# Optimization experiments

Hardware: AMD Instinct MI355X
Metric: run time of the kernel (lower is better)

Reference implementation:

```python
import jax, jax.numpy as jnp
import numpy as np
from jax import lax

B, H, W, C = 8, 128, 128, 256
HEADS, WIN, PRETRAIN = 8, 8, 8
QK_U = C // HEADS            # 32
QK_CH = QK_U * HEADS         # 256
KV_CH = QK_CH + C            # 512
BLOCK = WIN // 2             # key block size at half resolution
HALO = WIN                   # halo window (halo_window//2) at half resolution
PAD = (HALO - BLOCK) // 2    # halo overlap pad at half resolution


def _win_part(x, heads):
    b, h, w, c = x.shape
    u = c // heads
    x = x.reshape(b, h // WIN, WIN, w // WIN, WIN, heads, u)
    x = x.transpose(0, 1, 3, 5, 2, 4, 6)
    return x.reshape(b, (h // WIN) * (w // WIN), heads, WIN * WIN, u)


def _halo_part(x):
    # overlapping halo blocks: [b,hh,wh,c] -> [b, nw, HALO*HALO, c]
    b, h, w, c = x.shape
    xp = jnp.pad(x, ((0, 0), (PAD, PAD), (PAD, PAD), (0, 0)))
    hb, wb = h // BLOCK, w // BLOCK
    ih = jnp.arange(hb)[:, None] * BLOCK + jnp.arange(HALO)[None, :]
    iw = jnp.arange(wb)[:, None] * BLOCK + jnp.arange(HALO)[None, :]
    t = xp[:, ih][:, :, :, iw]            # [b, hb, HALO, wb, HALO, c]
    t = t.transpose(0, 1, 3, 2, 4, 5)
    return t.reshape(b, hb * wb, HALO * HALO, c)


def _halo_part_fused(x, heads):
    t = _halo_part(x)
    b, nw, l, c = t.shape
    u = c // heads
    return t.reshape(b, nw, l, heads, u).transpose(0, 1, 3, 2, 4)


def _l2n(x):
    # tf.math.l2_normalize with epsilon=1.55e-5
    return x * lax.rsqrt(jnp.maximum(jnp.sum(x * x, -1, keepdims=True), 1.55e-5))


def _rel_bias(cpb_w1, cpb_b1, cpb_w2):
    # Swin-V2 style continuous (log-CPB) relative bias between full-res query
    # window and half-res halo key window.
    qc = jnp.arange(WIN, dtype=jnp.float32)
    kc = (jnp.arange(HALO, dtype=jnp.float32) - PAD) * 2.0 + 0.5  # half-res centers in full-res coords
    r1 = qc[:, None] - kc[None, :]
    rel_y = jnp.broadcast_to(r1[:, None, :, None], (WIN, WIN, HALO, HALO))
    rel_x = jnp.broadcast_to(r1[None, :, None, :], (WIN, WIN, HALO, HALO))
    rel = jnp.stack([rel_y, rel_x], -1).reshape(WIN * WIN, HALO * HALO, 2)
    rel = rel / (PRETRAIN - 1) * 8.0
    rel = jnp.sign(rel) * jnp.log2(jnp.abs(rel) + 1.0) / np.float32(np.log2(8.0))
    hmid = jax.nn.relu(rel @ cpb_w1 + cpb_b1)
    bias = 16.0 * jax.nn.sigmoid(hmid @ cpb_w2)   # [q, k, heads]
    return bias.transpose(2, 0, 1)[None, None]    # [1,1,heads,q,k]


def _pad_mask(dtype):
    # No outer divisible-pad here (H,W divisible), but halo zero-padding at the
    # image border must be masked out (-100 on out-of-image key positions).
    m = jnp.ones((1, H // 2, W // 2, 1), dtype)   # min-pooled validity map (all ones)
    hm = _halo_part(m)                            # [1, nw, HALO*HALO, 1]; border halos -> 0
    return -100.0 * (hm[..., 0] == 0).astype(dtype)[:, :, None, None, :]  # [1,nw,1,1,k]


def reference(inputs, qkv_w, q_bias, v_bias, dw_w, dw_gamma, dw_beta, dw_mean, dw_var, scale, cpb_w1, cpb_b1, cpb_w2, proj_w, proj_b):
    qkv = jnp.einsum('bhwc,cd->bhwd', inputs, qkv_w)
    q, kv = qkv[..., :QK_CH], qkv[..., QK_CH:]
    # depthwise 3x3 stride-2 conv + (inference) batch-norm on K/V path
    kv = lax.conv_general_dilated(kv, dw_w, (2, 2), 'SAME',
                                  dimension_numbers=('NHWC', 'HWIO', 'NHWC'),
                                  feature_group_count=KV_CH)
    kv = (kv - dw_mean) * lax.rsqrt(dw_var + 1e-3) * dw_gamma + dw_beta
    q = q + q_bias
    kv = kv + jnp.concatenate([jnp.zeros_like(q_bias), v_bias])
    qw = _win_part(q, HEADS)                                 # [B,nw,h,64,QK_U]
    k = _halo_part_fused(kv[..., :QK_CH], HEADS)             # [B,nw,h,64,QK_U]
    v = _halo_part_fused(kv[..., QK_CH:], HEADS)             # [B,nw,h,64,V_U]
    logit_scale = jnp.exp(jnp.minimum(scale, np.float32(np.log(100.0))))  # [h,1,1]
    attn = jnp.einsum('bnhqd,bnhkd->bnhqk', _l2n(qw) * logit_scale, _l2n(k))
    attn = attn + _rel_bias(cpb_w1, cpb_b1, cpb_w2) + _pad_mask(attn.dtype)
    attn = jax.nn.softmax(attn, axis=-1)
    out = jnp.einsum('bnhqk,bnhkd->bnhqd', attn, v)
    hb, wb = H // WIN, W // WIN
    out = out.reshape(B, hb, wb, HEADS, WIN, WIN, C // HEADS)
    out = out.transpose(0, 1, 4, 2, 5, 3, 6).reshape(B, H, W, C)
    return jnp.einsum('bhwc,cd->bhwd', out, proj_w) + proj_b


def setup_inputs() -> dict:
    key = jax.random.key(0)
    ks = jax.random.split(key, 16)
    rn = lambda k, s, sc=0.05: jax.random.normal(k, s, jnp.float32) * sc
    return {
        'inputs': jax.random.normal(ks[0], (B, H, W, C), jnp.float32),
        'qkv_w': rn(ks[1], (C, 2 * QK_CH + C)),
        'q_bias': rn(ks[2], (QK_CH,)),
        'v_bias': rn(ks[3], (C,)),
        'dw_w': rn(ks[4], (3, 3, 1, KV_CH)),
        'dw_gamma': 1.0 + rn(ks[5], (KV_CH,)),
        'dw_beta': rn(ks[6], (KV_CH,)),
        'dw_mean': rn(ks[7], (KV_CH,)),
        'dw_var': jax.random.uniform(ks[8], (KV_CH,), jnp.float32, 0.5, 1.5),
        'scale': jnp.full((HEADS, 1, 1), np.log(10.0), jnp.float32),
        'cpb_w1': rn(ks[9], (2, 512), 0.5),
        'cpb_b1': rn(ks[10], (512,), 0.1),
        'cpb_w2': rn(ks[11], (512, HEADS), 0.1),
        'proj_w': rn(ks[12], (C, C)),
        'proj_b': rn(ks[13], (C,)),
    }
```

## Files before the change

kernel.cpp:

```cpp
#include <hip/hip_runtime.h>
#include <stdint.h>


typedef __attribute__((ext_vector_type(8))) short short8;
typedef __attribute__((ext_vector_type(4))) short short4v;
typedef __attribute__((ext_vector_type(4))) float f32x4;

__device__ __forceinline__ float bf2f(unsigned short u){
  union { unsigned int i; float f; } x; x.i = ((unsigned int)u)<<16; return x.f;
}
__device__ __forceinline__ unsigned short f2bf(float f){
  union { float f; unsigned int i; } x; x.f = f;
  unsigned int r = x.i + 0x7FFFu + ((x.i>>16)&1u);
  return (unsigned short)(r>>16);
}
__device__ __forceinline__ void gl_lds16(const void* g, void* l){
  __builtin_amdgcn_global_load_lds((const __attribute__((address_space(1))) unsigned int*)g,
                                   (__attribute__((address_space(3))) unsigned int*)l, 16, 0, 0);
}

__global__ __launch_bounds__(256) void cvt_bf16_kernel(const float* __restrict__ in,
                                                       short* __restrict__ out, long n8)
{
  long stride = (long)gridDim.x * 256;
  for (long i = (long)blockIdx.x*256 + threadIdx.x; i < n8; i += stride){
    float4 a = ((const float4*)in)[2*i];
    float4 b = ((const float4*)in)[2*i+1];
    short8 v;
    v[0]=(short)f2bf(a.x); v[1]=(short)f2bf(a.y); v[2]=(short)f2bf(a.z); v[3]=(short)f2bf(a.w);
    v[4]=(short)f2bf(b.x); v[5]=(short)f2bf(b.y); v[6]=(short)f2bf(b.z); v[7]=(short)f2bf(b.w);
    ((short8*)out)[i] = v;
  }
}

__global__ void transpose_w_kernel(const float* __restrict__ w, short* __restrict__ wt,
                                   int K, int N)
{
  int idx = blockIdx.x*256 + threadIdx.x;
  if (idx >= K*N) return;
  int n = idx / K, k = idx - n*K;
  wt[idx] = (short)f2bf(w[(long)k*N + n]);
}

__global__ __launch_bounds__(64) void relbias_kernel(const float* __restrict__ w1,
    const float* __restrict__ b1, const float* __restrict__ w2, float* __restrict__ out)
{
  int q = blockIdx.x;
  int k = threadIdx.x;
  float ry = (float)(q>>3) - (((float)(k>>3) - 2.f)*2.f + 0.5f);
  float rx = (float)(q&7)  - (((float)(k&7)  - 2.f)*2.f + 0.5f);
  ry *= (8.f/7.f); rx *= (8.f/7.f);
  float sy = (ry>0.f)?1.f:((ry<0.f)?-1.f:0.f);
  float sx = (rx>0.f)?1.f:((rx<0.f)?-1.f:0.f);
  ry = sy * log2f(fabsf(ry)+1.f) * (1.f/3.f);
  rx = sx * log2f(fabsf(rx)+1.f) * (1.f/3.f);
  float acc[8] = {0,0,0,0,0,0,0,0};
  for (int j=0;j<512;j++){
    float hm = ry*w1[j] + rx*w1[512+j] + b1[j];
    hm = fmaxf(hm, 0.f);
#pragma unroll
    for (int h=0;h<8;h++) acc[h] += hm * w2[j*8+h];
  }
#pragma unroll
  for (int h=0;h<8;h++)
    out[h*4096 + q*64 + k] = 16.f / (1.f + __expf(-acc[h]));
}

template<int ND, int OUTMODE>
__global__ __launch_bounds__(256) void gemm_bt_kernel(const short* __restrict__ A,
    const short* __restrict__ Bt, const float* __restrict__ bias,
    short* __restrict__ out_q, short* __restrict__ out_kv, float* __restrict__ out_f)
{
  __shared__ short smem[32768];
  const int tid  = threadIdx.x;
  const int lane = tid & 63;
  const int wid  = tid >> 6;
  const int wr = wid >> 1, wc = wid & 1;

  constexpr int NCB = ND / 128;
  const int bid = blockIdx.x;
  const int xcd = bid & 7;
  const int idx = bid >> 3;
  const long row0 = (long)(xcd * 128 + idx / NCB) * 128;
  const int  col0 = (idx % NCB) * 128;

  f32x4 acc[4][4];
#pragma unroll
  for (int m=0;m<4;m++)
#pragma unroll
    for (int n=0;n<4;n++) acc[m][n] = (f32x4){0.f,0.f,0.f,0.f};

  auto stage = [&](int buf, int kt){
#pragma unroll
    for (int j = 0; j < 4; j++) {
      int f = j*256 + tid;
      int r = f >> 3, p = f & 7;
      gl_lds16(A + (row0 + r)*256 + kt + ((p ^ (r&7))<<3),
               smem + buf*8192 + ((j*256 + (wid<<6))<<3));
      gl_lds16(Bt + (long)(col0 + r)*256 + kt + ((p ^ (r&7))<<3),
               smem + 16384 + buf*8192 + ((j*256 + (wid<<6))<<3));
    }
  };
  auto compute = [&](int buf){
    const short* As = smem + buf*8192;
    const short* Bs = smem + 16384 + buf*8192;
#pragma unroll
    for (int ks = 0; ks < 2; ks++) {
      short8 af[4], bfv[4];
#pragma unroll
      for (int m=0;m<4;m++){
        int r = wr*64 + m*16 + (lane & 15);
        int g = ks*4 + (lane >> 4);
        af[m] = *(const short8*)(As + r*64 + ((g ^ (r&7))<<3));
      }
#pragma unroll
      for (int n=0;n<4;n++){
        int r = wc*64 + n*16 + (lane & 15);
        int g = ks*4 + (lane >> 4);
        bfv[n] = *(const short8*)(Bs + r*64 + ((g ^ (r&7))<<3));
      }
#pragma unroll
      for (int m=0;m<4;m++)
#pragma unroll
        for (int n=0;n<4;n++)
          acc[m][n] = __builtin_amdgcn_mfma_f32_16x16x32_bf16(af[m], bfv[n], acc[m][n], 0, 0, 0);
    }
  };

  stage(0, 0);
  __syncthreads();
#pragma unroll
  for (int t = 0; t < 4; t++){
    if (t < 3) stage((t+1)&1, (t+1)*64);
    compute(t&1);
    __syncthreads();
  }

  if (OUTMODE == 0) {
    float bcol[4];
#pragma unroll
    for (int n=0;n<4;n++){
      int col = col0 + wc*64 + n*16 + (lane&15);
      bcol[n] = (col < 256) ? bias[col] : 0.f;
    }
#pragma unroll
    for (int m=0;m<4;m++){
#pragma unroll
      for (int n=0;n<4;n++){
        int col = wc*64 + n*16 + (lane&15);
        int cg = col >> 3;
#pragma unroll
        for (int rg=0;rg<4;rg++){
          int row = wr*64 + m*16 + ((lane>>4)<<2) + rg;
          smem[row*128 + ((cg ^ (row&7))<<3) + (col&7)] = (short)f2bf(acc[m][n][rg] + bcol[n]);
        }
      }
    }
    __syncthreads();
    int row = tid >> 1, ch = tid & 1;
    long grow = row0 + row;
#pragma unroll
    for (int j=0;j<8;j++){
      int cg = ch*8 + j;
      short8 v = *(const short8*)(smem + row*128 + ((cg ^ (row&7))<<3));
      int col = col0 + cg*8;
      if (col0 < 256) *(short8*)(out_q + grow*256 + col)        = v;
      else            *(short8*)(out_kv + grow*512 + (col-256)) = v;
    }
  } else {
    float* fs = (float*)smem;
#pragma unroll
    for (int m=0;m<4;m++){
#pragma unroll
      for (int n=0;n<4;n++){
        int col = wc*64 + n*16 + (lane&15);
        int c4 = col >> 2;
        float bv = bias[col0 + col];
#pragma unroll
        for (int rg=0;rg<4;rg++){
          int row = wr*64 + m*16 + ((lane>>4)<<2) + rg;
          fs[row*128 + ((c4 ^ (row&7))<<2) + (col&3)] = acc[m][n][rg] + bv;
        }
      }
    }
    __syncthreads();
    int row = tid >> 1;
    long grow = row0 + row;
#pragma unroll
    for (int j=0;j<16;j++){
      int c4 = (tid&1)*16 + j;
      float4 v = *(const float4*)(fs + row*128 + ((c4 ^ (row&7))<<2));
      *(float4*)(out_f + grow*ND + col0 + c4*4) = v;
    }
  }
}

__global__ __launch_bounds__(256) void dwconv_kernel(const short* __restrict__ kv_buf,
    const float* __restrict__ dw_w, const float* __restrict__ gamma,
    const float* __restrict__ beta, const float* __restrict__ mean,
    const float* __restrict__ var, const float* __restrict__ v_bias,
    short* __restrict__ kv_ds)
{
  const int bid = blockIdx.x;
  const int b  = bid >> 7;
  const int rem = bid & 127;
  const int y2 = rem >> 1, xq = rem & 1;
  const int tid = threadIdx.x;
  const int lane = tid & 63, w = tid >> 6;
  const int ch0 = lane * 8;

  float s[8], sh[8];
#pragma unroll
  for (int i=0;i<8;i+=4){
    float4 g4 = *(const float4*)(gamma + ch0 + i);
    float4 v4 = *(const float4*)(var   + ch0 + i);
    float4 m4 = *(const float4*)(mean  + ch0 + i);
    float4 b4 = *(const float4*)(beta  + ch0 + i);
    float gg[4] = {g4.x,g4.y,g4.z,g4.w}, vv[4] = {v4.x,v4.y,v4.z,v4.w};
    float mm[4] = {m4.x,m4.y,m4.z,m4.w}, bb[4] = {b4.x,b4.y,b4.z,b4.w};
#pragma unroll
    for (int j=0;j<4;j++){
      float sv = gg[j] * rsqrtf(vv[j] + 1e-3f);
      s[i+j]  = sv;
      sh[i+j] = bb[j] - mm[j]*sv;
    }
  }
  if (ch0 >= 256){
    float4 vb0 = *(const float4*)(v_bias + ch0 - 256);
    float4 vb1 = *(const float4*)(v_bias + ch0 - 252);
    sh[0]+=vb0.x; sh[1]+=vb0.y; sh[2]+=vb0.z; sh[3]+=vb0.w;
    sh[4]+=vb1.x; sh[5]+=vb1.y; sh[6]+=vb1.z; sh[7]+=vb1.w;
  }

  float wv[9][8];
#pragma unroll
  for (int t=0;t<9;t++){
    float4 w0 = *(const float4*)(dw_w + t*512 + ch0);
    float4 w1 = *(const float4*)(dw_w + t*512 + ch0 + 4);
    wv[t][0]=w0.x; wv[t][1]=w0.y; wv[t][2]=w0.z; wv[t][3]=w0.w;
    wv[t][4]=w1.x; wv[t][5]=w1.y; wv[t][6]=w1.z; wv[t][7]=w1.w;
  }

  const int y0 = y2*2;
  const bool vy2 = (y0 + 2) < 128;
  const short* r0 = kv_buf + (((long)b*128 + y0)*128)*512 + ch0;
  const short* r1 = r0 + 128*512;
  const short* r2 = r1 + 128*512;
  const short8 zero8 = {0,0,0,0,0,0,0,0};

  const int x2base = xq*32 + w*8;
  const int xs = x2base*2;

  auto ld = [&](const short* r, int x, bool vy)->short8 {
    if (vy && x < 128) return *(const short8*)(r + (long)x*512);
    return zero8;
  };

  short8 L0 = ld(r0, xs, true), L1 = ld(r1, xs, true), L2 = ld(r2, xs, vy2);

#pragma unroll
  for (int i=0;i<8;i++){
    const int x2 = x2base + i;
    const int xm = xs + 2*i + 1, xr = xs + 2*i + 2;
    short8 M0 = ld(r0, xm, true), M1 = ld(r1, xm, true), M2 = ld(r2, xm, vy2);
    short8 R0 = ld(r0, xr, true), R1 = ld(r1, xr, true), R2 = ld(r2, xr, vy2);

    float acc[8];
#pragma unroll
    for (int c=0;c<8;c++) acc[c] = 0.f;
#pragma unroll
    for (int c=0;c<8;c++){
      acc[c] += bf2f((unsigned short)L0[c]) * wv[0][c];
      acc[c] += bf2f((unsigned short)M0[c]) * wv[1][c];
      acc[c] += bf2f((unsigned short)R0[c]) * wv[2][c];
      acc[c] += bf2f((unsigned short)L1[c]) * wv[3][c];
      acc[c] += bf2f((unsigned short)M1[c]) * wv[4][c];
      acc[c] += bf2f((unsigned short)R1[c]) * wv[5][c];
      acc[c] += bf2f((unsigned short)L2[c]) * wv[6][c];
      acc[c] += bf2f((unsigned short)M2[c]) * wv[7][c];
      acc[c] += bf2f((unsigned short)R2[c]) * wv[8][c];
    }
    short8 o;
#pragma unroll
    for (int c=0;c<8;c++) o[c] = (short)f2bf(acc[c]*s[c] + sh[c]);
    *(short8*)(kv_ds + ((long)((b*64+y2)*64 + x2))*512 + ch0) = o;

    L0 = R0; L1 = R1; L2 = R2;
  }
}

__global__ __launch_bounds__(256) void halo_attn_kernel(const short* __restrict__ q_buf,
    const short* __restrict__ kv_ds, const float* __restrict__ relb,
    const float* __restrict__ scale, short* __restrict__ attn_out)
{
  __shared__ float qss[8][64];
  __shared__ float kss[8][64];
  __shared__ short vts[4][32][72];
  __shared__ short ps [4][64][72];

  const int bid = blockIdx.x;
  const int b = bid >> 8, wno = bid & 255;
  const int bi = wno >> 4, bj = wno & 15;
  const int tid = threadIdx.x;
  const int w = tid >> 6, lane = tid & 63;

#pragma unroll
  for (int i=0;i<4;i++){
    int idx = i*256 + tid;
    int isk = idx >> 9;
    int h   = (idx >> 6) & 7;
    int row = idx & 63;
    float ss = 0.f;
    if (!isk) {
      int qy = row>>3, qx = row&7;
      const short* p = q_buf + ((long)((b*128 + bi*8 + qy)*128 + (bj*8+qx)))*256 + h*32;
#pragma unroll
      for (int j=0;j<4;j++){
        short8 v = *(const short8*)(p + j*8);
#pragma unroll
        for (int e=0;e<8;e++){ float f = bf2f((unsigned short)v[e]); ss += f*f; }
      }
      qss[h][row] = fmaxf(ss, 1.55e-5f);
    } else {
      int ky = row>>3, kx = row&7;
      int yy = bi*4 - 2 + ky, xx = bj*4 - 2 + kx;
      if (yy>=0 && yy<64 && xx>=0 && xx<64) {
        const short* p = kv_ds + ((long)((b*64+yy)*64+xx))*512 + h*32;
#pragma unroll
        for (int j=0;j<4;j++){
          short8 v = *(const short8*)(p + j*8);
#pragma unroll
          for (int e=0;e<8;e++){ float f = bf2f((unsigned short)v[e]); ss += f*f; }
        }
      }
      kss[h][row] = fmaxf(ss, 1.55e-5f);
    }
  }
  __syncthreads();

  const short8 zero8 = {0,0,0,0,0,0,0,0};

  for (int hi=0; hi<2; hi++){
    int h = w + hi*4;
    float lscale = __expf(fminf(scale[h], 4.6051702f));

#pragma unroll 4
    for (int j=0;j<32;j++){
      int flat = j*64 + lane;
      int key = flat >> 5, d = flat & 31;
      int ky = key>>3, kx = key&7;
      int yy = bi*4-2+ky, xx = bj*4-2+kx;
      short val = 0;
      if (yy>=0 && yy<64 && xx>=0 && xx<64)
        val = kv_ds[((long)((b*64+yy)*64+xx))*512 + 256 + h*32 + d];
      vts[w][d][key] = val;
    }

    short8 af[4], bfv[4];
#pragma unroll
    for (int m=0;m<4;m++){
      int key = m*16 + (lane&15);
      int ky = key>>3, kx = key&7;
      int yy = bi*4-2+ky, xx = bj*4-2+kx;
      if (yy>=0 && yy<64 && xx>=0 && xx<64)
        af[m] = *(const short8*)(kv_ds + ((long)((b*64+yy)*64+xx))*512 + h*32 + ((lane>>4)<<3));
      else
        af[m] = zero8;
    }
#pragma unroll
    for (int n=0;n<4;n++){
      int q = n*16 + (lane&15);
      int qy = q>>3, qx = q&7;
      bfv[n] = *(const short8*)(q_buf + ((long)((b*128+bi*8+qy)*128 + bj*8+qx))*256 + h*32 + ((lane>>4)<<3));
    }
    f32x4 sc_[4][4];
#pragma unroll
    for (int m=0;m<4;m++)
#pragma unroll
      for (int n=0;n<4;n++)
        sc_[m][n] = __builtin_amdgcn_mfma_f32_16x16x32_bf16(af[m], bfv[n],
                        (f32x4){0.f,0.f,0.f,0.f}, 0, 0, 0);

    float rq[4];
#pragma unroll
    for (int n=0;n<4;n++) rq[n] = rsqrtf(qss[h][n*16 + (lane&15)]);
    float mx[4] = {-1e30f,-1e30f,-1e30f,-1e30f};
#pragma unroll
    for (int m=0;m<4;m++){
      int key0 = m*16 + ((lane>>4)<<2);
      float rk[4], mk[4];
#pragma unroll
      for (int r=0;r<4;r++){
        int key = key0 + r;
        int ky = key>>3, kx = key&7;
        int yy = bi*4-2+ky, xx = bj*4-2+kx;
        rk[r] = rsqrtf(kss[h][key]);
        mk[r] = (yy>=0 && yy<64 && xx>=0 && xx<64) ? 0.f : -100.f;
      }
#pragma unroll
      for (int n=0;n<4;n++){
        int q = n*16 + (lane&15);
        f32x4 rb = *(const f32x4*)(relb + h*4096 + q*64 + key0);
#pragma unroll
        for (int r=0;r<4;r++){
          float v = sc_[m][n][r] * (rk[r]*rq[n]*lscale) + rb[r] + mk[r];
          sc_[m][n][r] = v;
          mx[n] = fmaxf(mx[n], v);
        }
      }
    }
#pragma unroll
    for (int n=0;n<4;n++){
      mx[n] = fmaxf(mx[n], __shfl_xor(mx[n], 16));
      mx[n] = fmaxf(mx[n], __shfl_xor(mx[n], 32));
    }
    float sm[4] = {0.f,0.f,0.f,0.f};
#pragma unroll
    for (int m=0;m<4;m++)
#pragma unroll
      for (int n=0;n<4;n++)
#pragma unroll
        for (int r=0;r<4;r++){
          float e = __expf(sc_[m][n][r] - mx[n]);
          sc_[m][n][r] = e;
          sm[n] += e;
        }
#pragma unroll
    for (int n=0;n<4;n++){
      sm[n] += __shfl_xor(sm[n], 16);
      sm[n] += __shfl_xor(sm[n], 32);
      sm[n] = 1.f / sm[n];
    }
#pragma unroll
    for (int n=0;n<4;n++){
      int q = n*16 + (lane&15);
#pragma unroll
      for (int m=0;m<4;m++){
        short4v pk;
#pragma unroll
        for (int r=0;r<4;r++) pk[r] = (short)f2bf(sc_[m][n][r] * sm[n]);
        *(short4v*)(&ps[w][q][m*16 + ((lane>>4)<<2)]) = pk;
      }
    }
    __syncthreads();

    f32x4 oc[4][2];
#pragma unroll
    for (int m=0;m<4;m++)
#pragma unroll
      for (int n=0;n<2;n++) oc[m][n] = (f32x4){0.f,0.f,0.f,0.f};
#pragma unroll
    for (int ks=0; ks<2; ks++){
      short8 pa[4], vb[2];
#pragma unroll
      for (int m=0;m<4;m++)
        pa[m] = *(const short8*)(&ps[w][m*16 + (lane&15)][ks*32 + ((lane>>4)<<3)]);
#pragma unroll
      for (int n=0;n<2;n++)
        vb[n] = *(const short8*)(&vts[w][n*16 + (lane&15)][ks*32 + ((lane>>4)<<3)]);
#pragma unroll
      for (int m=0;m<4;m++)
#pragma unroll
        for (int n=0;n<2;n++)
          oc[m][n] = __builtin_amdgcn_mfma_f32_16x16x32_bf16(pa[m], vb[n], oc[m][n], 0, 0, 0);
    }
#pragma unroll
    for (int m=0;m<4;m++){
      int q0 = m*16 + ((lane>>4)<<2);
#pragma unroll
      for (int n=0;n<2;n++){
        int d = n*16 + (lane&15);
#pragma unroll
        for (int r=0;r<4;r++){
          int q = q0 + r;
          int qy = q>>3, qx = q&7;
          attn_out[((long)((b*128 + bi*8+qy)*128 + bj*8+qx))*256 + h*32 + d] =
              (short)f2bf(oc[m][n][r]);
        }
      }
    }
    __syncthreads();
  }
}

extern "C" void kernel_launch(void* const* d_in, const int* in_sizes, int n_in,
                              void* d_out, int out_size, void* d_ws, size_t ws_size,
                              hipStream_t stream)
{
  (void)in_sizes; (void)n_in; (void)out_size; (void)ws_size;
  const float* inputs = (const float*)d_in[0];
  const float* qkv_w  = (const float*)d_in[1];
  const float* q_bias = (const float*)d_in[2];
  const float* v_bias = (const float*)d_in[3];
  const float* dw_w   = (const float*)d_in[4];
  const float* dw_g   = (const float*)d_in[5];
  const float* dw_b   = (const float*)d_in[6];
  const float* dw_m   = (const float*)d_in[7];
  const float* dw_v   = (const float*)d_in[8];
  const float* scale  = (const float*)d_in[9];
  const float* cpb_w1 = (const float*)d_in[10];
  const float* cpb_b1 = (const float*)d_in[11];
  const float* cpb_w2 = (const float*)d_in[12];
  const float* proj_w = (const float*)d_in[13];
  const float* proj_b = (const float*)d_in[14];

  char* ws = (char*)d_ws;
  short* q_buf    = (short*)(ws);
  short* kv_buf   = (short*)(ws + 67108864L);
  short* kv_ds    = (short*)(ws + 201326592L);
  short* attn_buf = (short*)(ws + 234881024L);
  short* qkvw_t   = (short*)(ws + 301989888L);
  short* projw_t  = (short*)(ws + 302383104L);
  float* relb     = (float*)(ws + 302514176L);

  short* a_bf = attn_buf;

  cvt_bf16_kernel<<<2048, 256, 0, stream>>>(inputs, a_bf, 4194304L);
  transpose_w_kernel<<<768, 256, 0, stream>>>(qkv_w, qkvw_t, 256, 768);
  transpose_w_kernel<<<256, 256, 0, stream>>>(proj_w, projw_t, 256, 256);
  relbias_kernel<<<64, 64, 0, stream>>>(cpb_w1, cpb_b1, cpb_w2, relb);

  gemm_bt_kernel<768, 0><<<6144, 256, 0, stream>>>(
      a_bf, qkvw_t, q_bias, q_buf, kv_buf, nullptr);

  dwconv_kernel<<<1024, 256, 0, stream>>>(kv_buf, dw_w, dw_g, dw_b, dw_m, dw_v, v_bias, kv_ds);

  halo_attn_kernel<<<2048, 256, 0, stream>>>(q_buf, kv_ds, relb, scale, attn_buf);

  gemm_bt_kernel<256, 1><<<2048, 256, 0, stream>>>(
      attn_buf, projw_t, proj_b, nullptr, nullptr, (float*)d_out);
}
```

Before: 454.6 us.

## Store V transposed and padded, compute QK norms in-register in halo attention

The depthwise-conv kernel now writes K to its own compact buffer and V to a per-head, per-channel transposed plane padded by two pixels on each side. Halo attention can then load V fragments straight from global memory into MFMA operands, with no LDS staging and no bounds checks. The separate Q/K sum-of-squares pass and its LDS arrays are replaced by per-lane partial sums reduced with shuffles. Softmax uses exp2 with log2(e) folded into the scale and the relative bias, and normalization is deferred to the output. The P tile uses a per-wave swizzled LDS buffer without block barriers. The cost is scattered 2-byte V stores in dwconv, and the padded V border is never written, so correctness relies on the workspace already holding zeros there.

```diff
diff --git a/kernel.cpp b/kernel.cpp
--- a/kernel.cpp
+++ b/kernel.cpp
@@ -5,6 +5,8 @@
 typedef __attribute__((ext_vector_type(8))) short short8;
 typedef __attribute__((ext_vector_type(4))) short short4v;
 typedef __attribute__((ext_vector_type(4))) float f32x4;
+
+#define VT_PLANE 4624L
 
 __device__ __forceinline__ float bf2f(unsigned short u){
   union { unsigned int i; float f; } x; x.i = ((unsigned int)u)<<16; return x.f;
@@ -13,6 +15,10 @@
   union { float f; unsigned int i; } x; x.f = f;
   unsigned int r = x.i + 0x7FFFu + ((x.i>>16)&1u);
   return (unsigned short)(r>>16);
+}
+__device__ __forceinline__ unsigned int pack_bf_t(float a, float b){
+  union { float f; unsigned int u; } x, y; x.f = a; y.f = b;
+  return (y.u & 0xFFFF0000u) | (x.u >> 16);
 }
 __device__ __forceinline__ void gl_lds16(const void* g, void* l){
   __builtin_amdgcn_global_load_lds((const __attribute__((address_space(1))) unsigned int*)g,
@@ -63,7 +69,7 @@
   }
 #pragma unroll
   for (int h=0;h<8;h++)
-    out[h*4096 + q*64 + k] = 16.f / (1.f + __expf(-acc[h]));
+    out[h*4096 + q*64 + k] = (16.f / (1.f + __expf(-acc[h]))) * 1.4426950408889634f;
 }
 
 template<int ND, int OUTMODE>
@@ -199,7 +205,7 @@
     const float* __restrict__ dw_w, const float* __restrict__ gamma,
     const float* __restrict__ beta, const float* __restrict__ mean,
     const float* __restrict__ var, const float* __restrict__ v_bias,
-    short* __restrict__ kv_ds)
+    short* __restrict__ kv_K, short* __restrict__ v_t)
 {
   const int bid = blockIdx.x;
   const int b  = bid >> 7;
@@ -257,6 +263,9 @@
   };
 
   short8 L0 = ld(r0, xs, true), L1 = ld(r1, xs, true), L2 = ld(r2, xs, vy2);
+
+  const int vc = ch0 - 256, hh = vc >> 5, d0 = vc & 31;
+  const long vtb = ((long)((b*8+hh)*32 + d0))*VT_PLANE + (long)(y2+2)*68;
 
 #pragma unroll
   for (int i=0;i<8;i++){
@@ -283,128 +292,121 @@
     short8 o;
 #pragma unroll
     for (int c=0;c<8;c++) o[c] = (short)f2bf(acc[c]*s[c] + sh[c]);
-    *(short8*)(kv_ds + ((long)((b*64+y2)*64 + x2))*512 + ch0) = o;
-
+
+    if (ch0 < 256) {
+      *(short8*)(kv_K + ((long)((b*64+y2)*64 + x2))*256 + ch0) = o;
+    } else {
+      long base = vtb + (x2+2);
+#pragma unroll
+      for (int c=0;c<8;c++) v_t[base + (long)c*VT_PLANE] = o[c];
+    }
     L0 = R0; L1 = R1; L2 = R2;
   }
 }
 
 __global__ __launch_bounds__(256) void halo_attn_kernel(const short* __restrict__ q_buf,
-    const short* __restrict__ kv_ds, const float* __restrict__ relb,
-    const float* __restrict__ scale, short* __restrict__ attn_out)
-{
-  __shared__ float qss[8][64];
-  __shared__ float kss[8][64];
-  __shared__ short vts[4][32][72];
-  __shared__ short ps [4][64][72];
+    const short* __restrict__ kv_K, const short* __restrict__ v_t,
+    const float* __restrict__ relb, const float* __restrict__ scale,
+    short* __restrict__ attn_out)
+{
+  __shared__ short ps[4][4096];
 
   const int bid = blockIdx.x;
   const int b = bid >> 8, wno = bid & 255;
   const int bi = wno >> 4, bj = wno & 15;
   const int tid = threadIdx.x;
   const int w = tid >> 6, lane = tid & 63;
-
-#pragma unroll
-  for (int i=0;i<4;i++){
-    int idx = i*256 + tid;
-    int isk = idx >> 9;
-    int h   = (idx >> 6) & 7;
-    int row = idx & 63;
-    float ss = 0.f;
-    if (!isk) {
-      int qy = row>>3, qx = row&7;
-      const short* p = q_buf + ((long)((b*128 + bi*8 + qy)*128 + (bj*8+qx)))*256 + h*32;
-#pragma unroll
-      for (int j=0;j<4;j++){
-        short8 v = *(const short8*)(p + j*8);
-#pragma unroll
-        for (int e=0;e<8;e++){ float f = bf2f((unsigned short)v[e]); ss += f*f; }
-      }
-      qss[h][row] = fmaxf(ss, 1.55e-5f);
-    } else {
-      int ky = row>>3, kx = row&7;
-      int yy = bi*4 - 2 + ky, xx = bj*4 - 2 + kx;
-      if (yy>=0 && yy<64 && xx>=0 && xx<64) {
-        const short* p = kv_ds + ((long)((b*64+yy)*64+xx))*512 + h*32;
-#pragma unroll
-        for (int j=0;j<4;j++){
-          short8 v = *(const short8*)(p + j*8);
-#pragma unroll
-          for (int e=0;e<8;e++){ float f = bf2f((unsigned short)v[e]); ss += f*f; }
-        }
-      }
-      kss[h][row] = fmaxf(ss, 1.55e-5f);
-    }
-  }
-  __syncthreads();
-
+  const int g = lane >> 4, q15 = lane & 15;
+  short* myps = &ps[w][0];
   const short8 zero8 = {0,0,0,0,0,0,0,0};
 
+  long kbase[4]; bool kval[4];
+#pragma unroll
+  for (int m=0;m<4;m++){
+    int key = m*16 + q15;
+    int yy = bi*4-2 + (key>>3), xx = bj*4-2 + (key&7);
+    kval[m] = (yy>=0 && yy<64 && xx>=0 && xx<64);
+    kbase[m] = ((long)((b*64+yy)*64+xx))*256 + g*8;
+  }
+  float mkv[4][4];
+#pragma unroll
+  for (int m=0;m<4;m++)
+#pragma unroll
+    for (int r=0;r<4;r++){
+      int key = m*16 + g*4 + r;
+      int yy = bi*4-2+(key>>3), xx = bj*4-2+(key&7);
+      mkv[m][r] = (yy>=0&&yy<64&&xx>=0&&xx<64) ? 0.f : -30000.f;
+    }
+  long qpix[4];
+#pragma unroll
+  for (int n=0;n<4;n++){
+    int q = n*16+q15;
+    qpix[n] = ((long)((b*128+bi*8+(q>>3))*128 + bj*8+(q&7)))*256;
+  }
+  int voff[2];
+#pragma unroll
+  for (int ks=0;ks<2;ks++) voff[ks] = (bi*4+ks*4+g)*68 + bj*4;
+
   for (int hi=0; hi<2; hi++){
-    int h = w + hi*4;
-    float lscale = __expf(fminf(scale[h], 4.6051702f));
-
-#pragma unroll 4
-    for (int j=0;j<32;j++){
-      int flat = j*64 + lane;
-      int key = flat >> 5, d = flat & 31;
-      int ky = key>>3, kx = key&7;
-      int yy = bi*4-2+ky, xx = bj*4-2+kx;
-      short val = 0;
-      if (yy>=0 && yy<64 && xx>=0 && xx<64)
-        val = kv_ds[((long)((b*64+yy)*64+xx))*512 + 256 + h*32 + d];
-      vts[w][d][key] = val;
-    }
-
-    short8 af[4], bfv[4];
+    const int h = w + hi*4;
+    const float lsc = __expf(fminf(scale[h], 4.6051702f)) * 1.4426950408889634f;
+
+    short8 va[2][2];
+#pragma unroll
+    for (int dblk=0;dblk<2;dblk++){
+      long pl = ((long)((b*8+h)*32 + dblk*16 + q15))*VT_PLANE;
+#pragma unroll
+      for (int ks=0;ks<2;ks++)
+        va[dblk][ks] = *(const short8*)(v_t + pl + voff[ks]);
+    }
+
+    short8 af[4]; float rkk[4];
 #pragma unroll
     for (int m=0;m<4;m++){
-      int key = m*16 + (lane&15);
-      int ky = key>>3, kx = key&7;
-      int yy = bi*4-2+ky, xx = bj*4-2+kx;
-      if (yy>=0 && yy<64 && xx>=0 && xx<64)
-        af[m] = *(const short8*)(kv_ds + ((long)((b*64+yy)*64+xx))*512 + h*32 + ((lane>>4)<<3));
-      else
-        af[m] = zero8;
-    }
+      af[m] = kval[m] ? *(const short8*)(kv_K + kbase[m] + h*32) : zero8;
+      float ss = 0.f;
+#pragma unroll
+      for (int e=0;e<8;e++){ float f = bf2f((unsigned short)af[m][e]); ss += f*f; }
+      ss += __shfl_xor(ss, 16);
+      ss += __shfl_xor(ss, 32);
+      rkk[m] = rsqrtf(fmaxf(ss, 1.55e-5f));
+    }
+    short8 bfv[4]; float rq[4];
 #pragma unroll
     for (int n=0;n<4;n++){
-      int q = n*16 + (lane&15);
-      int qy = q>>3, qx = q&7;
-      bfv[n] = *(const short8*)(q_buf + ((long)((b*128+bi*8+qy)*128 + bj*8+qx))*256 + h*32 + ((lane>>4)<<3));
-    }
-    f32x4 sc_[4][4];
+      bfv[n] = *(const short8*)(q_buf + qpix[n] + h*32 + g*8);
+      float ss = 0.f;
+#pragma unroll
+      for (int e=0;e<8;e++){ float f = bf2f((unsigned short)bfv[n][e]); ss += f*f; }
+      ss += __shfl_xor(ss, 16);
+      ss += __shfl_xor(ss, 32);
+      rq[n] = rsqrtf(fmaxf(ss, 1.55e-5f)) * lsc;
+    }
+    float rk[4][4];
 #pragma unroll
     for (int m=0;m<4;m++)
 #pragma unroll
+      for (int r=0;r<4;r++)
+        rk[m][r] = __shfl(rkk[m], ((lane>>4)<<2) + r);
+
+    f32x4 sc[4][4];
+#pragma unroll
+    for (int m=0;m<4;m++)
+#pragma unroll
       for (int n=0;n<4;n++)
-        sc_[m][n] = __builtin_amdgcn_mfma_f32_16x16x32_bf16(af[m], bfv[n],
-                        (f32x4){0.f,0.f,0.f,0.f}, 0, 0, 0);
-
-    float rq[4];
-#pragma unroll
-    for (int n=0;n<4;n++) rq[n] = rsqrtf(qss[h][n*16 + (lane&15)]);
-    float mx[4] = {-1e30f,-1e30f,-1e30f,-1e30f};
+        sc[m][n] = __builtin_amdgcn_mfma_f32_16x16x32_bf16(af[m], bfv[n],
+                       (f32x4){0.f,0.f,0.f,0.f}, 0, 0, 0);
+
+    float mx[4] = {-3e38f,-3e38f,-3e38f,-3e38f};
 #pragma unroll
     for (int m=0;m<4;m++){
-      int key0 = m*16 + ((lane>>4)<<2);
-      float rk[4], mk[4];
-#pragma unroll
-      for (int r=0;r<4;r++){
-        int key = key0 + r;
-        int ky = key>>3, kx = key&7;
-        int yy = bi*4-2+ky, xx = bj*4-2+kx;
-        rk[r] = rsqrtf(kss[h][key]);
-        mk[r] = (yy>=0 && yy<64 && xx>=0 && xx<64) ? 0.f : -100.f;
-      }
 #pragma unroll
       for (int n=0;n<4;n++){
-        int q = n*16 + (lane&15);
-        f32x4 rb = *(const f32x4*)(relb + h*4096 + q*64 + key0);
+        f32x4 rb = *(const f32x4*)(relb + h*4096 + (n*16+q15)*64 + m*16 + g*4);
 #pragma unroll
         for (int r=0;r<4;r++){
-          float v = sc_[m][n][r] * (rk[r]*rq[n]*lscale) + rb[r] + mk[r];
-          sc_[m][n][r] = v;
+          float v = sc[m][n][r] * (rk[m][r]*rq[n]) + rb[r] + mkv[m][r];
+          sc[m][n][r] = v;
           mx[n] = fmaxf(mx[n], v);
         }
       }
@@ -421,65 +423,59 @@
       for (int n=0;n<4;n++)
 #pragma unroll
         for (int r=0;r<4;r++){
-          float e = __expf(sc_[m][n][r] - mx[n]);
-          sc_[m][n][r] = e;
+          float e = exp2f(sc[m][n][r] - mx[n]);
+          sc[m][n][r] = e;
           sm[n] += e;
         }
+    float sminv[4];
 #pragma unroll
     for (int n=0;n<4;n++){
       sm[n] += __shfl_xor(sm[n], 16);
       sm[n] += __shfl_xor(sm[n], 32);
-      sm[n] = 1.f / sm[n];
-    }
+      sminv[n] = 1.f / sm[n];
+    }
+
 #pragma unroll
     for (int n=0;n<4;n++){
-      int q = n*16 + (lane&15);
+      int row = n*16 + q15;
 #pragma unroll
       for (int m=0;m<4;m++){
-        short4v pk;
-#pragma unroll
-        for (int r=0;r<4;r++) pk[r] = (short)f2bf(sc_[m][n][r] * sm[n]);
-        *(short4v*)(&ps[w][q][m*16 + ((lane>>4)<<2)]) = pk;
-      }
-    }
-    __syncthreads();
-
-    f32x4 oc[4][2];
-#pragma unroll
-    for (int m=0;m<4;m++)
-#pragma unroll
-      for (int n=0;n<2;n++) oc[m][n] = (f32x4){0.f,0.f,0.f,0.f};
-#pragma unroll
-    for (int ks=0; ks<2; ks++){
-      short8 pa[4], vb[2];
-#pragma unroll
-      for (int m=0;m<4;m++)
-        pa[m] = *(const short8*)(&ps[w][m*16 + (lane&15)][ks*32 + ((lane>>4)<<3)]);
-#pragma unroll
-      for (int n=0;n<2;n++)
-        vb[n] = *(const short8*)(&vts[w][n*16 + (lane&15)][ks*32 + ((lane>>4)<<3)]);
-#pragma unroll
-      for (int m=0;m<4;m++)
-#pragma unroll
-        for (int n=0;n<2;n++)
-          oc[m][n] = __builtin_amdgcn_mfma_f32_16x16x32_bf16(pa[m], vb[n], oc[m][n], 0, 0, 0);
-    }
-#pragma unroll
-    for (int m=0;m<4;m++){
-      int q0 = m*16 + ((lane>>4)<<2);
-#pragma unroll
-      for (int n=0;n<2;n++){
-        int d = n*16 + (lane&15);
-#pragma unroll
-        for (int r=0;r<4;r++){
-          int q = q0 + r;
-          int qy = q>>3, qx = q&7;
-          attn_out[((long)((b*128 + bi*8+qy)*128 + bj*8+qx))*256 + h*32 + d] =
-              (short)f2bf(oc[m][n][r]);
-        }
-      }
-    }
-    __syncthreads();
+        uint2 pk;
+        pk.x = pack_bf_t(sc[m][n][0], sc[m][n][1]);
+        pk.y = pack_bf_t(sc[m][n][2], sc[m][n][3]);
+        int kc = (m*2 + (g>>1)) ^ (row & 7);
+        *(uint2*)(myps + row*64 + kc*8 + ((g&1)<<2)) = pk;
+      }
+    }
+    asm volatile("s_waitcnt lgkmcnt(0)" ::: "memory");
+
+    f32x4 oc[2][4];
+#pragma unroll
+    for (int dblk=0;dblk<2;dblk++)
+#pragma unroll
+      for (int n=0;n<4;n++) oc[dblk][n] = (f32x4){0.f,0.f,0.f,0.f};
+#pragma unroll
+    for (int ks=0;ks<2;ks++){
+#pragma unroll
+      for (int n=0;n<4;n++){
+        int row = n*16 + q15;
+        short8 pb = *(const short8*)(myps + row*64 + (((ks*4+g) ^ (row&7))<<3));
+#pragma unroll
+        for (int dblk=0;dblk<2;dblk++)
+          oc[dblk][n] = __builtin_amdgcn_mfma_f32_16x16x32_bf16(va[dblk][ks], pb, oc[dblk][n], 0, 0, 0);
+      }
+    }
+
+#pragma unroll
+    for (int dblk=0;dblk<2;dblk++){
+#pragma unroll
+      for (int n=0;n<4;n++){
+        uint2 pk;
+        pk.x = pack_bf_t(oc[dblk][n][0]*sminv[n], oc[dblk][n][1]*sminv[n]);
+        pk.y = pack_bf_t(oc[dblk][n][2]*sminv[n], oc[dblk][n][3]*sminv[n]);
+        *(uint2*)(attn_out + qpix[n] + h*32 + dblk*16 + g*4) = pk;
+      }
+    }
   }
 }
 
@@ -507,11 +503,12 @@
   char* ws = (char*)d_ws;
   short* q_buf    = (short*)(ws);
   short* kv_buf   = (short*)(ws + 67108864L);
-  short* kv_ds    = (short*)(ws + 201326592L);
-  short* attn_buf = (short*)(ws + 234881024L);
-  short* qkvw_t   = (short*)(ws + 301989888L);
-  short* projw_t  = (short*)(ws + 302383104L);
-  float* relb     = (float*)(ws + 302514176L);
+  short* kv_K     = (short*)(ws + 201326592L);
+  short* v_t      = (short*)(ws + 218103808L);
+  short* attn_buf = (short*)(ws + 237043712L);
+  short* qkvw_t   = (short*)(ws + 304152576L);
+  short* projw_t  = (short*)(ws + 304939008L);
+  float* relb     = (float*)(ws + 305070080L);
 
   short* a_bf = attn_buf;
 
@@ -523,9 +520,10 @@
   gemm_bt_kernel<768, 0><<<6144, 256, 0, stream>>>(
       a_bf, qkvw_t, q_bias, q_buf, kv_buf, nullptr);
 
-  dwconv_kernel<<<1024, 256, 0, stream>>>(kv_buf, dw_w, dw_g, dw_b, dw_m, dw_v, v_bias, kv_ds);
-
-  halo_attn_kernel<<<2048, 256, 0, stream>>>(q_buf, kv_ds, relb, scale, attn_buf);
+  dwconv_kernel<<<1024, 256, 0, stream>>>(kv_buf, dw_w, dw_g, dw_b, dw_m, dw_v, v_bias,
+                                          kv_K, v_t);
+
+  halo_attn_kernel<<<2048, 256, 0, stream>>>(q_buf, kv_K, v_t, relb, scale, attn_buf);
 
   gemm_bt_kernel<256, 1><<<2048, 256, 0, stream>>>(
       attn_buf, projw_t, proj_b, nullptr, nullptr, (float*)d_out);
```

After: 467.3 us. 1.03x slower.
